# Optimization experiments

Measured on AMD Instinct MI355X. Metric: run time of the kernel, lower is better.

Reference implementation:

```python
import jax, jax.numpy as jnp
import numpy as np

N = 100000      # nodes
E = 1600000     # edges (avg degree 16)
D_IN = 128
CONV_SIZES = [64, 64]
FC_SIZES = [64, 32, 1]


def _glorot(key, shape):
    lim = np.sqrt(6.0 / (shape[0] + shape[1]))
    return jax.random.uniform(key, shape, jnp.float32, -lim, lim)


def setup_inputs() -> dict:
    key = jax.random.key(0)
    ks = jax.random.split(key, 2 + len(CONV_SIZES) + len(FC_SIZES))
    inp = {
        "x": jax.random.normal(ks[0], (N, D_IN), jnp.float32),
        "edge_index": jax.random.randint(ks[1], (2, E), 0, N, dtype=jnp.int64),
    }
    size = D_IN
    ki = 2
    for li, s in enumerate(CONV_SIZES):
        inp[f"cW{li}"] = _glorot(ks[ki], (size, s)); ki += 1
        inp[f"cb{li}"] = jnp.zeros((s,), jnp.float32)
        size = s
    for li, s in enumerate(FC_SIZES):
        inp[f"fW{li}"] = _glorot(ks[ki], (size, s)); ki += 1
        inp[f"fb{li}"] = jnp.zeros((s,), jnp.float32)
        size = s
    return inp


def gcn_conv(x, src, dst, W, b, n_nodes):
    """PyG GCNConv: symmetric normalization with added self-loops."""
    xl = x @ W  # [N, out]
    # degree including self-loop
    deg = jnp.zeros((n_nodes,), xl.dtype).at[dst].add(1.0) + 1.0
    dinv = jax.lax.rsqrt(deg)
    norm = dinv[src] * dinv[dst]                 # [E]
    msg = xl[src] * norm[:, None]                # gather + scale, [E, out]
    agg = jax.ops.segment_sum(msg, dst, num_segments=n_nodes)
    # self-loop contribution: norm = 1/deg
    return agg + xl * (1.0 / deg)[:, None] + b


def reference(x, edge_index, cW0, cb0, cW1, cb1, fW0, fb0, fW1, fb1, fW2, fb2):
    src, dst = edge_index[0], edge_index[1]
    h = jnp.tanh(gcn_conv(x, src, dst, cW0, cb0, N))
    h = jnp.tanh(gcn_conv(h, src, dst, cW1, cb1, N))
    h = jnp.tanh(h @ fW0 + fb0)
    h = jnp.tanh(h @ fW1 + fb1)
    return h @ fW2 + fb2  # [N, 1]
```

## Files before the change

### kernel.cpp

```cpp
#include <hip/hip_runtime.h>
#include <math.h>

#define N_NODES 100000
#define N_EDGES 1600000
#define NB     391
#define CHUNK  4096
#define NBLK_A 391

typedef unsigned short ushort_t;

__device__ inline unsigned short f2bf(float f) {
    unsigned u = __float_as_uint(f);
    unsigned r = (u + 0x7FFFu + ((u >> 16) & 1u)) >> 16;
    return (unsigned short)r;
}
__device__ inline void acc2(float& a0, float& a1, unsigned u) {
    a0 += __uint_as_float(u << 16);
    a1 += __uint_as_float(u & 0xFFFF0000u);
}
__device__ inline float fast_tanh(float x) {
    float e = __expf(2.0f * x);
    return fmaf(-2.0f, __builtin_amdgcn_rcpf(e + 1.0f), 1.0f);
}
__device__ inline void fma4(float4& acc, const float4 a,
                            const float4 w0, const float4 w1,
                            const float4 w2, const float4 w3) {
    acc.x = fmaf(a.x, w0.x, fmaf(a.y, w1.x, fmaf(a.z, w2.x, fmaf(a.w, w3.x, acc.x))));
    acc.y = fmaf(a.x, w0.y, fmaf(a.y, w1.y, fmaf(a.z, w2.y, fmaf(a.w, w3.y, acc.y))));
    acc.z = fmaf(a.x, w0.z, fmaf(a.y, w1.z, fmaf(a.z, w2.z, fmaf(a.w, w3.z, acc.z))));
    acc.w = fmaf(a.x, w0.w, fmaf(a.y, w1.w, fmaf(a.z, w2.w, fmaf(a.w, w3.w, acc.w))));
}
__device__ inline void bf8_to_f32(float* p, uint4 v) {
    p[0] = __uint_as_float(v.x << 16); p[1] = __uint_as_float(v.x & 0xFFFF0000u);
    p[2] = __uint_as_float(v.y << 16); p[3] = __uint_as_float(v.y & 0xFFFF0000u);
    p[4] = __uint_as_float(v.z << 16); p[5] = __uint_as_float(v.z & 0xFFFF0000u);
    p[6] = __uint_as_float(v.w << 16); p[7] = __uint_as_float(v.w & 0xFFFF0000u);
}


__global__ __launch_bounds__(256) void k_count(const int* __restrict__ dst,
                                               unsigned* __restrict__ cnt) {
    __shared__ unsigned h[NB];
    const int tid = threadIdx.x;
    const long e0 = (long)blockIdx.x * CHUNK;
    for (int i = tid; i < NB; i += 256) h[i] = 0u;
    __syncthreads();
    for (int i = tid; i < CHUNK; i += 256) {
        long e = e0 + i;
        if (e < N_EDGES) atomicAdd(&h[((unsigned)dst[e]) >> 8], 1u);
    }
    __syncthreads();
    for (int b = tid; b < NB; b += 256) cnt[b * NBLK_A + blockIdx.x] = h[b];
}

__global__ __launch_bounds__(512) void k_bucket_scan(unsigned* __restrict__ cnt,
                                                     unsigned* __restrict__ btot) {
    __shared__ unsigned s[512];
    const int tid = threadIdx.x;
    const int b = blockIdx.x;
    unsigned v = (tid < NBLK_A) ? cnt[b * NBLK_A + tid] : 0u;
    s[tid] = v;
    __syncthreads();
    for (int o = 1; o < 512; o <<= 1) {
        unsigned t = (tid >= o) ? s[tid - o] : 0u;
        __syncthreads();
        s[tid] += t;
        __syncthreads();
    }
    if (tid < NBLK_A) cnt[b * NBLK_A + tid] = s[tid] - v;
    if (tid == NBLK_A - 1) btot[b] = s[tid];
}

__global__ __launch_bounds__(512) void k_scan_bkt(const unsigned* __restrict__ btot,
                                                  unsigned* __restrict__ bktbase) {
    __shared__ unsigned s[512];
    const int tid = threadIdx.x;
    unsigned v = (tid < NB) ? btot[tid] : 0u;
    s[tid] = v;
    __syncthreads();
    for (int o = 1; o < 512; o <<= 1) {
        unsigned t = (tid >= o) ? s[tid - o] : 0u;
        __syncthreads();
        s[tid] += t;
        __syncthreads();
    }
    if (tid < NB) bktbase[tid] = s[tid] - v;
    if (tid == NB - 1) bktbase[NB] = s[tid];
}

__global__ __launch_bounds__(256) void k_bin(const int* __restrict__ src,
                                             const int* __restrict__ dst,
                                             const unsigned* __restrict__ cnt,
                                             const unsigned* __restrict__ bktbase,
                                             unsigned* __restrict__ binned) {
    __shared__ unsigned cntA[NB];
    __shared__ unsigned excl[NB];
    __shared__ unsigned gbase[NB];
    __shared__ unsigned scanbuf[512];
    __shared__ unsigned data[CHUNK];
    const int tid = threadIdx.x;
    const long e0 = (long)blockIdx.x * CHUNK;

    for (int i = tid; i < NB; i += 256) cntA[i] = 0u;
    __syncthreads();
    for (int i = tid; i < CHUNK; i += 256) {
        long e = e0 + i;
        if (e < N_EDGES) atomicAdd(&cntA[((unsigned)dst[e]) >> 8], 1u);
    }
    __syncthreads();
    scanbuf[tid] = (tid < NB) ? cntA[tid] : 0u;
    scanbuf[tid + 256] = (tid + 256 < NB) ? cntA[tid + 256] : 0u;
    __syncthreads();
    for (int o = 1; o < 512; o <<= 1) {
        unsigned v0 = (tid >= o) ? scanbuf[tid - o] : 0u;
        unsigned v1 = (tid + 256 >= o) ? scanbuf[tid + 256 - o] : 0u;
        __syncthreads();
        scanbuf[tid] += v0;
        scanbuf[tid + 256] += v1;
        __syncthreads();
    }
    for (int b = tid; b < NB; b += 256) {
        excl[b] = scanbuf[b] - cntA[b];
        gbase[b] = bktbase[b] + cnt[b * NBLK_A + blockIdx.x];
    }
    __syncthreads();
    for (int i = tid; i < NB; i += 256) cntA[i] = 0u;
    __syncthreads();
    for (int i = tid; i < CHUNK; i += 256) {
        long e = e0 + i;
        if (e < N_EDGES) {
            unsigned d = (unsigned)dst[e];
            unsigned b = d >> 8;
            unsigned slot = excl[b] + atomicAdd(&cntA[b], 1u);
            data[slot] = (((unsigned)src[e]) << 8) | (d & 255u);
        }
    }
    __syncthreads();
    const int w = tid >> 6, lane = tid & 63;
    for (int b = w; b < NB; b += 4) {
        unsigned c = cntA[b];
        unsigned sb = excl[b], gb = gbase[b];
        for (unsigned k = lane; k < c; k += 64)
            binned[gb + k] = data[sb + k];
    }
}

__global__ __launch_bounds__(256) void k_csr_fill2(const unsigned* __restrict__ binned,
                                                   const unsigned* __restrict__ bktbase,
                                                   unsigned* __restrict__ rowptr,
                                                   float* __restrict__ dinv,
                                                   int* __restrict__ ssrc) {
    __shared__ unsigned cnt[256];
    __shared__ unsigned s[256];
    __shared__ unsigned cur[256];
    const int b = blockIdx.x;
    const int tid = threadIdx.x;
    const int n0 = b * 256;
    const unsigned beg = bktbase[b], end = bktbase[b + 1];
    cnt[tid] = 0u;
    __syncthreads();
    for (unsigned i = beg + tid; i < end; i += 256)
        atomicAdd(&cnt[binned[i] & 255u], 1u);
    __syncthreads();
    const unsigned v = cnt[tid];
    s[tid] = v;
    __syncthreads();
    for (int o = 1; o < 256; o <<= 1) {
        unsigned t = (tid >= o) ? s[tid - o] : 0u;
        __syncthreads();
        s[tid] += t;
        __syncthreads();
    }
    const unsigned excl = s[tid] - v;
    const int node = n0 + tid;
    if (node < N_NODES) {
        rowptr[node] = beg + excl;
        dinv[node] = rsqrtf((float)(v + 1u));
        if (node == N_NODES - 1) rowptr[N_NODES] = end;
    }
    cur[tid] = beg + excl;
    __syncthreads();
    for (unsigned i = beg + tid; i < end; i += 256) {
        unsigned p = binned[i];
        unsigned pos = atomicAdd(&cur[p & 255u], 1u);
        ssrc[pos] = (int)(p >> 8);
    }
}


template<int K>
__global__ __launch_bounds__(256) void k_gemm_bf(const float* __restrict__ A,
                                                 const float* __restrict__ W,
                                                 const float* __restrict__ dinv,
                                                 ushort_t* __restrict__ C) {
    constexpr int OUT = 64;
    constexpr int BR = 64;
    constexpr int LDA = K + 4;
    __shared__ float Wld[K * OUT];
    __shared__ float Ald[BR * LDA];
    const int tid = threadIdx.x;
    const int row0 = blockIdx.x * BR;
    const int nrows = (N_NODES - row0 < BR) ? (N_NODES - row0) : BR;

    {
        const float4* W4 = reinterpret_cast<const float4*>(W);
        float4* Wl4 = reinterpret_cast<float4*>(Wld);
        for (int i = tid; i < K * OUT / 4; i += 256) Wl4[i] = W4[i];
        const float4* A4 = reinterpret_cast<const float4*>(A + (size_t)row0 * K);
        const int nv = nrows * (K / 4);
        for (int i = tid; i < nv; i += 256) {
            int r = i / (K / 4), q = i % (K / 4);
            *reinterpret_cast<float4*>(&Ald[r * LDA + q * 4]) = A4[i];
        }
    }
    __syncthreads();

    const int tr = tid >> 4;
    const int tc = tid & 15;
    const int r0 = tr * 4;
    float4 acc0 = {0,0,0,0}, acc1 = {0,0,0,0}, acc2v = {0,0,0,0}, acc3 = {0,0,0,0};
#pragma unroll 2
    for (int k4 = 0; k4 < K; k4 += 4) {
        const float4 a0 = *reinterpret_cast<const float4*>(&Ald[(r0 + 0) * LDA + k4]);
        const float4 a1 = *reinterpret_cast<const float4*>(&Ald[(r0 + 1) * LDA + k4]);
        const float4 a2 = *reinterpret_cast<const float4*>(&Ald[(r0 + 2) * LDA + k4]);
        const float4 a3 = *reinterpret_cast<const float4*>(&Ald[(r0 + 3) * LDA + k4]);
        const float4 w0 = *reinterpret_cast<const float4*>(&Wld[(k4 + 0) * OUT + tc * 4]);
        const float4 w1 = *reinterpret_cast<const float4*>(&Wld[(k4 + 1) * OUT + tc * 4]);
        const float4 w2 = *reinterpret_cast<const float4*>(&Wld[(k4 + 2) * OUT + tc * 4]);
        const float4 w3 = *reinterpret_cast<const float4*>(&Wld[(k4 + 3) * OUT + tc * 4]);
        fma4(acc0, a0, w0, w1, w2, w3);
        fma4(acc1, a1, w0, w1, w2, w3);
        fma4(acc2v, a2, w0, w1, w2, w3);
        fma4(acc3, a3, w0, w1, w2, w3);
    }
    float4 accs[4] = {acc0, acc1, acc2v, acc3};
#pragma unroll
    for (int i = 0; i < 4; ++i) {
        const int r = r0 + i;
        if (r < nrows) {
            const float di = dinv[row0 + r];
            ushort4 o;
            o.x = f2bf(accs[i].x * di);
            o.y = f2bf(accs[i].y * di);
            o.z = f2bf(accs[i].z * di);
            o.w = f2bf(accs[i].w * di);
            *reinterpret_cast<ushort4*>(&C[(size_t)(row0 + r) * 64 + tc * 4]) = o;
        }
    }
}

__global__ __launch_bounds__(256) void k_gemm_bfin(const ushort_t* __restrict__ A,
                                                   const float* __restrict__ W,
                                                   const float* __restrict__ dinv,
                                                   ushort_t* __restrict__ C) {
    constexpr int K = 64;
    constexpr int OUT = 64;
    constexpr int BR = 64;
    constexpr int LDA = K + 4;
    __shared__ float Wld[K * OUT];
    __shared__ float Ald[BR * LDA];
    const int tid = threadIdx.x;
    const int row0 = blockIdx.x * BR;
    const int nrows = (N_NODES - row0 < BR) ? (N_NODES - row0) : BR;

    {
        const float4* W4 = reinterpret_cast<const float4*>(W);
        float4* Wl4 = reinterpret_cast<float4*>(Wld);
        for (int i = tid; i < K * OUT / 4; i += 256) Wl4[i] = W4[i];
        const uint4* A4 = reinterpret_cast<const uint4*>(A + (size_t)row0 * K);
        const int nv = nrows * 8;
        for (int i = tid; i < nv; i += 256) {
            int r = i >> 3, q = i & 7;
            bf8_to_f32(&Ald[r * LDA + q * 8], A4[i]);
        }
    }
    __syncthreads();

    const int tr = tid >> 4;
    const int tc = tid & 15;
    const int r0 = tr * 4;
    float4 acc0 = {0,0,0,0}, acc1 = {0,0,0,0}, acc2v = {0,0,0,0}, acc3 = {0,0,0,0};
#pragma unroll 2
    for (int k4 = 0; k4 < K; k4 += 4) {
        const float4 a0 = *reinterpret_cast<const float4*>(&Ald[(r0 + 0) * LDA + k4]);
        const float4 a1 = *reinterpret_cast<const float4*>(&Ald[(r0 + 1) * LDA + k4]);
        const float4 a2 = *reinterpret_cast<const float4*>(&Ald[(r0 + 2) * LDA + k4]);
        const float4 a3 = *reinterpret_cast<const float4*>(&Ald[(r0 + 3) * LDA + k4]);
        const float4 w0 = *reinterpret_cast<const float4*>(&Wld[(k4 + 0) * OUT + tc * 4]);
        const float4 w1 = *reinterpret_cast<const float4*>(&Wld[(k4 + 1) * OUT + tc * 4]);
        const float4 w2 = *reinterpret_cast<const float4*>(&Wld[(k4 + 2) * OUT + tc * 4]);
        const float4 w3 = *reinterpret_cast<const float4*>(&Wld[(k4 + 3) * OUT + tc * 4]);
        fma4(acc0, a0, w0, w1, w2, w3);
        fma4(acc1, a1, w0, w1, w2, w3);
        fma4(acc2v, a2, w0, w1, w2, w3);
        fma4(acc3, a3, w0, w1, w2, w3);
    }
    float4 accs[4] = {acc0, acc1, acc2v, acc3};
#pragma unroll
    for (int i = 0; i < 4; ++i) {
        const int r = r0 + i;
        if (r < nrows) {
            const float di = dinv[row0 + r];
            ushort4 o;
            o.x = f2bf(accs[i].x * di);
            o.y = f2bf(accs[i].y * di);
            o.z = f2bf(accs[i].z * di);
            o.w = f2bf(accs[i].w * di);
            *reinterpret_cast<ushort4*>(&C[(size_t)(row0 + r) * 64 + tc * 4]) = o;
        }
    }
}

__global__ __launch_bounds__(256) void k_agg(const ushort_t* __restrict__ xlb,
                                             const float* __restrict__ dinv,
                                             const unsigned* __restrict__ rowptr,
                                             const int* __restrict__ ssrc,
                                             const float* __restrict__ bias,
                                             ushort_t* __restrict__ hb) {
    const int node = blockIdx.x * 4 + (threadIdx.x >> 6);
    const int lane = threadIdx.x & 63;
    const int g = lane >> 3;
    const int l = lane & 7;
    const uint4* xb4 = reinterpret_cast<const uint4*>(xlb);

    const unsigned beg = rowptr[node], end = rowptr[node + 1];
    float a[8] = {0.f,0.f,0.f,0.f,0.f,0.f,0.f,0.f};
    float b[8] = {0.f,0.f,0.f,0.f,0.f,0.f,0.f,0.f};
    if (g == 0) {
        const uint4 v = xb4[(size_t)node * 8 + l];
        acc2(a[0], a[1], v.x); acc2(a[2], a[3], v.y);
        acc2(a[4], a[5], v.z); acc2(a[6], a[7], v.w);
    }
    unsigned j = beg + g;
    for (; j + 8 < end; j += 16) {
        const int s0 = ssrc[j];
        const int s1 = ssrc[j + 8];
        const uint4 v0 = xb4[(size_t)s0 * 8 + l];
        const uint4 v1 = xb4[(size_t)s1 * 8 + l];
        acc2(a[0], a[1], v0.x); acc2(a[2], a[3], v0.y);
        acc2(a[4], a[5], v0.z); acc2(a[6], a[7], v0.w);
        acc2(b[0], b[1], v1.x); acc2(b[2], b[3], v1.y);
        acc2(b[4], b[5], v1.z); acc2(b[6], b[7], v1.w);
    }
    if (j < end) {
        const uint4 v = xb4[(size_t)ssrc[j] * 8 + l];
        acc2(a[0], a[1], v.x); acc2(a[2], a[3], v.y);
        acc2(a[4], a[5], v.z); acc2(a[6], a[7], v.w);
    }
#pragma unroll
    for (int i = 0; i < 8; ++i) a[i] += b[i];
#pragma unroll
    for (int i = 0; i < 8; ++i) {
        a[i] += __shfl_xor(a[i], 8);
        a[i] += __shfl_xor(a[i], 16);
        a[i] += __shfl_xor(a[i], 32);
    }
    if (g == 0) {
        const float di = dinv[node];
        const float4 b0 = reinterpret_cast<const float4*>(bias)[l * 2];
        const float4 b1 = reinterpret_cast<const float4*>(bias)[l * 2 + 1];
        float r0 = fast_tanh(fmaf(a[0], di, b0.x));
        float r1 = fast_tanh(fmaf(a[1], di, b0.y));
        float r2 = fast_tanh(fmaf(a[2], di, b0.z));
        float r3 = fast_tanh(fmaf(a[3], di, b0.w));
        float r4 = fast_tanh(fmaf(a[4], di, b1.x));
        float r5 = fast_tanh(fmaf(a[5], di, b1.y));
        float r6 = fast_tanh(fmaf(a[6], di, b1.z));
        float r7 = fast_tanh(fmaf(a[7], di, b1.w));
        uint4 o;
        o.x = (unsigned)f2bf(r0) | ((unsigned)f2bf(r1) << 16);
        o.y = (unsigned)f2bf(r2) | ((unsigned)f2bf(r3) << 16);
        o.z = (unsigned)f2bf(r4) | ((unsigned)f2bf(r5) << 16);
        o.w = (unsigned)f2bf(r6) | ((unsigned)f2bf(r7) << 16);
        reinterpret_cast<uint4*>(hb)[(size_t)node * 8 + l] = o;
    }
}

__global__ __launch_bounds__(256, 4) void k_fc(const ushort_t* __restrict__ h2,
                                               const float* __restrict__ fW0, const float* __restrict__ fb0,
                                               const float* __restrict__ fW1, const float* __restrict__ fb1,
                                               const float* __restrict__ fW2, const float* __restrict__ fb2,
                                               float* __restrict__ out) {
    constexpr int BR = 32;
    constexpr int LDH = 68;
    __shared__ float W0[64 * 64];
    __shared__ float W1[64 * 32];
    __shared__ float Hin[BR * LDH];
    __shared__ float Ht[BR * LDH];
    __shared__ float Hs[BR * 33];
    __shared__ float W2s[33];
    const int tid = threadIdx.x;
    {
        const float4* w04 = reinterpret_cast<const float4*>(fW0);
        float4* W04 = reinterpret_cast<float4*>(W0);
        for (int i = tid; i < 64 * 16; i += 256) W04[i] = w04[i];
        const float4* w14 = reinterpret_cast<const float4*>(fW1);
        float4* W14 = reinterpret_cast<float4*>(W1);
        for (int i = tid; i < 64 * 8; i += 256) W14[i] = w14[i];
        if (tid < 32) W2s[tid] = fW2[tid];
        if (tid == 32) W2s[32] = fb2[0];
    }
    const long row0 = (long)blockIdx.x * BR;
    {
        const uint4* H4 = reinterpret_cast<const uint4*>(h2 + row0 * 64);
        if (tid < BR * 8) {
            int r = tid >> 3, q = tid & 7;
            bf8_to_f32(&Hin[r * LDH + q * 8], H4[tid]);
        }
    }
    __syncthreads();

    {
        const int rp = tid >> 4;
        const int cq = tid & 15;
        const int r0 = rp * 2, r1 = r0 + 1;
        const float4 bias = reinterpret_cast<const float4*>(fb0)[cq];
        float4 acc0 = bias, acc1 = bias;
#pragma unroll 2
        for (int k4 = 0; k4 < 64; k4 += 4) {
            const float4 a0 = *reinterpret_cast<const float4*>(&Hin[r0 * LDH + k4]);
            const float4 a1 = *reinterpret_cast<const float4*>(&Hin[r1 * LDH + k4]);
            const float4 w0 = *reinterpret_cast<const float4*>(&W0[(k4 + 0) * 64 + cq * 4]);
            const float4 w1 = *reinterpret_cast<const float4*>(&W0[(k4 + 1) * 64 + cq * 4]);
            const float4 w2 = *reinterpret_cast<const float4*>(&W0[(k4 + 2) * 64 + cq * 4]);
            const float4 w3 = *reinterpret_cast<const float4*>(&W0[(k4 + 3) * 64 + cq * 4]);
            fma4(acc0, a0, w0, w1, w2, w3);
            fma4(acc1, a1, w0, w1, w2, w3);
        }
        float4 t0, t1;
        t0.x = fast_tanh(acc0.x); t0.y = fast_tanh(acc0.y);
        t0.z = fast_tanh(acc0.z); t0.w = fast_tanh(acc0.w);
        t1.x = fast_tanh(acc1.x); t1.y = fast_tanh(acc1.y);
        t1.z = fast_tanh(acc1.z); t1.w = fast_tanh(acc1.w);
        *reinterpret_cast<float4*>(&Ht[r0 * LDH + cq * 4]) = t0;
        *reinterpret_cast<float4*>(&Ht[r1 * LDH + cq * 4]) = t1;
    }
    __syncthreads();

    {
        const int r = tid >> 3;
        const int cq = tid & 7;
        const float4 bias = reinterpret_cast<const float4*>(fb1)[cq];
        float4 acc0 = bias;
#pragma unroll 2
        for (int k4 = 0; k4 < 64; k4 += 4) {
            const float4 a0 = *reinterpret_cast<const float4*>(&Ht[r * LDH + k4]);
            const float4 w0 = *reinterpret_cast<const float4*>(&W1[(k4 + 0) * 32 + cq * 4]);
            const float4 w1 = *reinterpret_cast<const float4*>(&W1[(k4 + 1) * 32 + cq * 4]);
            const float4 w2 = *reinterpret_cast<const float4*>(&W1[(k4 + 2) * 32 + cq * 4]);
            const float4 w3 = *reinterpret_cast<const float4*>(&W1[(k4 + 3) * 32 + cq * 4]);
            fma4(acc0, a0, w0, w1, w2, w3);
        }
        Hs[r * 33 + cq * 4 + 0] = fast_tanh(acc0.x);
        Hs[r * 33 + cq * 4 + 1] = fast_tanh(acc0.y);
        Hs[r * 33 + cq * 4 + 2] = fast_tanh(acc0.z);
        Hs[r * 33 + cq * 4 + 3] = fast_tanh(acc0.w);
    }
    __syncthreads();

    if (tid < BR) {
        float a = W2s[32];
        for (int k = 0; k < 32; ++k) a = fmaf(Hs[tid * 33 + k], W2s[k], a);
        out[row0 + tid] = a;
    }
}


extern "C" void kernel_launch(void* const* d_in, const int* in_sizes, int n_in,
                              void* d_out, int out_size, void* d_ws, size_t ws_size,
                              hipStream_t stream) {
    const float* x    = (const float*)d_in[0];
    const int*   eidx = (const int*)d_in[1];
    const float* cW0  = (const float*)d_in[2];
    const float* cb0  = (const float*)d_in[3];
    const float* cW1  = (const float*)d_in[4];
    const float* cb1  = (const float*)d_in[5];
    const float* fW0  = (const float*)d_in[6];
    const float* fb0  = (const float*)d_in[7];
    const float* fW1  = (const float*)d_in[8];
    const float* fb1  = (const float*)d_in[9];
    const float* fW2  = (const float*)d_in[10];
    const float* fb2  = (const float*)d_in[11];
    float* out = (float*)d_out;

    const int* src = eidx;
    const int* dst = eidx + N_EDGES;

    char* ws = (char*)d_ws;
    unsigned* rowptr  = (unsigned*)(ws);
    float*    dinv    = (float*)   (ws + 400016);
    unsigned* cnt     = (unsigned*)(ws + 800016);
    unsigned* btot    = (unsigned*)(ws + 1411552);
    unsigned* bktbase = (unsigned*)(ws + 1413120);
    int*      ssrc    = (int*)     (ws + 1414688);
    ushort_t* xlb     = (ushort_t*)(ws + 7814688);
    unsigned* binned  = (unsigned*)(ws + 20614688);
    ushort_t* hb      = (ushort_t*)(ws + 27014688);

    const int gRow = N_NODES / 32;
    const int gGemm = (N_NODES + 63) / 64;
    const int gAgg = N_NODES / 4;

    k_count<<<NBLK_A, 256, 0, stream>>>(dst, cnt);
    k_bucket_scan<<<NB, 512, 0, stream>>>(cnt, btot);
    k_scan_bkt<<<1, 512, 0, stream>>>(btot, bktbase);
    k_bin<<<NBLK_A, 256, 0, stream>>>(src, dst, cnt, bktbase, binned);
    k_csr_fill2<<<NB, 256, 0, stream>>>(binned, bktbase, rowptr, dinv, ssrc);

    k_gemm_bf<128><<<gGemm, 256, 0, stream>>>(x, cW0, dinv, xlb);
    k_agg<<<gAgg, 256, 0, stream>>>(xlb, dinv, rowptr, ssrc, cb0, hb);
    k_gemm_bfin<<<gGemm, 256, 0, stream>>>(hb, cW1, dinv, xlb);
    k_agg<<<gAgg, 256, 0, stream>>>(xlb, dinv, rowptr, ssrc, cb1, hb);
    k_fc<<<gRow, 256, 0, stream>>>(hb, fW0, fb0, fW1, fb1, fW2, fb2, out);
}
```

Measured before the change: 249.8 us.

## Fuse first GEMM with edge counting and defer degree scaling to aggregation

The first-layer GEMM no longer depends on dinv, so it is launched together with the edge-count histogram in one grid: extra blocks do the counting while the rest compute x@W0. The source-side dinv scaling is moved into a templated aggregation kernel that gathers dinv[src] per edge. The binning kernel now scatters its output with a per-slot bucket index instead of a per-bucket wave loop. This drops one kernel launch and overlaps the GEMM with the CSR build, at the cost of an extra scalar gather per edge in the first aggregation.

```diff
diff --git a/kernel.cpp b/kernel.cpp
--- a/kernel.cpp
+++ b/kernel.cpp
@@ -6,6 +6,7 @@
 #define NB     391
 #define CHUNK  4096
 #define NBLK_A 391
+#define GEMM0_BLOCKS 1563
 
 typedef unsigned short ushort_t;
 
@@ -17,6 +18,10 @@
 __device__ inline void acc2(float& a0, float& a1, unsigned u) {
     a0 += __uint_as_float(u << 16);
     a1 += __uint_as_float(u & 0xFFFF0000u);
+}
+__device__ inline void acc2s(float& a0, float& a1, unsigned u, float s) {
+    a0 = fmaf(__uint_as_float(u << 16), s, a0);
+    a1 = fmaf(__uint_as_float(u & 0xFFFF0000u), s, a1);
 }
 __device__ inline float fast_tanh(float x) {
     float e = __expf(2.0f * x);
@@ -37,171 +42,34 @@
     p[6] = __uint_as_float(v.w << 16); p[7] = __uint_as_float(v.w & 0xFFFF0000u);
 }
 
-
-__global__ __launch_bounds__(256) void k_count(const int* __restrict__ dst,
-                                               unsigned* __restrict__ cnt) {
-    __shared__ unsigned h[NB];
-    const int tid = threadIdx.x;
-    const long e0 = (long)blockIdx.x * CHUNK;
-    for (int i = tid; i < NB; i += 256) h[i] = 0u;
-    __syncthreads();
-    for (int i = tid; i < CHUNK; i += 256) {
-        long e = e0 + i;
-        if (e < N_EDGES) atomicAdd(&h[((unsigned)dst[e]) >> 8], 1u);
-    }
-    __syncthreads();
-    for (int b = tid; b < NB; b += 256) cnt[b * NBLK_A + blockIdx.x] = h[b];
-}
-
-__global__ __launch_bounds__(512) void k_bucket_scan(unsigned* __restrict__ cnt,
-                                                     unsigned* __restrict__ btot) {
-    __shared__ unsigned s[512];
-    const int tid = threadIdx.x;
-    const int b = blockIdx.x;
-    unsigned v = (tid < NBLK_A) ? cnt[b * NBLK_A + tid] : 0u;
-    s[tid] = v;
-    __syncthreads();
-    for (int o = 1; o < 512; o <<= 1) {
-        unsigned t = (tid >= o) ? s[tid - o] : 0u;
-        __syncthreads();
-        s[tid] += t;
-        __syncthreads();
-    }
-    if (tid < NBLK_A) cnt[b * NBLK_A + tid] = s[tid] - v;
-    if (tid == NBLK_A - 1) btot[b] = s[tid];
-}
-
-__global__ __launch_bounds__(512) void k_scan_bkt(const unsigned* __restrict__ btot,
-                                                  unsigned* __restrict__ bktbase) {
-    __shared__ unsigned s[512];
-    const int tid = threadIdx.x;
-    unsigned v = (tid < NB) ? btot[tid] : 0u;
-    s[tid] = v;
-    __syncthreads();
-    for (int o = 1; o < 512; o <<= 1) {
-        unsigned t = (tid >= o) ? s[tid - o] : 0u;
-        __syncthreads();
-        s[tid] += t;
-        __syncthreads();
-    }
-    if (tid < NB) bktbase[tid] = s[tid] - v;
-    if (tid == NB - 1) bktbase[NB] = s[tid];
-}
-
-__global__ __launch_bounds__(256) void k_bin(const int* __restrict__ src,
-                                             const int* __restrict__ dst,
-                                             const unsigned* __restrict__ cnt,
-                                             const unsigned* __restrict__ bktbase,
-                                             unsigned* __restrict__ binned) {
-    __shared__ unsigned cntA[NB];
-    __shared__ unsigned excl[NB];
-    __shared__ unsigned gbase[NB];
-    __shared__ unsigned scanbuf[512];
-    __shared__ unsigned data[CHUNK];
-    const int tid = threadIdx.x;
-    const long e0 = (long)blockIdx.x * CHUNK;
-
-    for (int i = tid; i < NB; i += 256) cntA[i] = 0u;
-    __syncthreads();
-    for (int i = tid; i < CHUNK; i += 256) {
-        long e = e0 + i;
-        if (e < N_EDGES) atomicAdd(&cntA[((unsigned)dst[e]) >> 8], 1u);
-    }
-    __syncthreads();
-    scanbuf[tid] = (tid < NB) ? cntA[tid] : 0u;
-    scanbuf[tid + 256] = (tid + 256 < NB) ? cntA[tid + 256] : 0u;
-    __syncthreads();
-    for (int o = 1; o < 512; o <<= 1) {
-        unsigned v0 = (tid >= o) ? scanbuf[tid - o] : 0u;
-        unsigned v1 = (tid + 256 >= o) ? scanbuf[tid + 256 - o] : 0u;
-        __syncthreads();
-        scanbuf[tid] += v0;
-        scanbuf[tid + 256] += v1;
-        __syncthreads();
-    }
-    for (int b = tid; b < NB; b += 256) {
-        excl[b] = scanbuf[b] - cntA[b];
-        gbase[b] = bktbase[b] + cnt[b * NBLK_A + blockIdx.x];
-    }
-    __syncthreads();
-    for (int i = tid; i < NB; i += 256) cntA[i] = 0u;
-    __syncthreads();
-    for (int i = tid; i < CHUNK; i += 256) {
-        long e = e0 + i;
-        if (e < N_EDGES) {
-            unsigned d = (unsigned)dst[e];
-            unsigned b = d >> 8;
-            unsigned slot = excl[b] + atomicAdd(&cntA[b], 1u);
-            data[slot] = (((unsigned)src[e]) << 8) | (d & 255u);
-        }
-    }
-    __syncthreads();
-    const int w = tid >> 6, lane = tid & 63;
-    for (int b = w; b < NB; b += 4) {
-        unsigned c = cntA[b];
-        unsigned sb = excl[b], gb = gbase[b];
-        for (unsigned k = lane; k < c; k += 64)
-            binned[gb + k] = data[sb + k];
-    }
-}
-
-__global__ __launch_bounds__(256) void k_csr_fill2(const unsigned* __restrict__ binned,
-                                                   const unsigned* __restrict__ bktbase,
-                                                   unsigned* __restrict__ rowptr,
-                                                   float* __restrict__ dinv,
-                                                   int* __restrict__ ssrc) {
-    __shared__ unsigned cnt[256];
-    __shared__ unsigned s[256];
-    __shared__ unsigned cur[256];
-    const int b = blockIdx.x;
-    const int tid = threadIdx.x;
-    const int n0 = b * 256;
-    const unsigned beg = bktbase[b], end = bktbase[b + 1];
-    cnt[tid] = 0u;
-    __syncthreads();
-    for (unsigned i = beg + tid; i < end; i += 256)
-        atomicAdd(&cnt[binned[i] & 255u], 1u);
-    __syncthreads();
-    const unsigned v = cnt[tid];
-    s[tid] = v;
-    __syncthreads();
-    for (int o = 1; o < 256; o <<= 1) {
-        unsigned t = (tid >= o) ? s[tid - o] : 0u;
-        __syncthreads();
-        s[tid] += t;
-        __syncthreads();
-    }
-    const unsigned excl = s[tid] - v;
-    const int node = n0 + tid;
-    if (node < N_NODES) {
-        rowptr[node] = beg + excl;
-        dinv[node] = rsqrtf((float)(v + 1u));
-        if (node == N_NODES - 1) rowptr[N_NODES] = end;
-    }
-    cur[tid] = beg + excl;
-    __syncthreads();
-    for (unsigned i = beg + tid; i < end; i += 256) {
-        unsigned p = binned[i];
-        unsigned pos = atomicAdd(&cur[p & 255u], 1u);
-        ssrc[pos] = (int)(p >> 8);
-    }
-}
-
-
-template<int K>
-__global__ __launch_bounds__(256) void k_gemm_bf(const float* __restrict__ A,
-                                                 const float* __restrict__ W,
-                                                 const float* __restrict__ dinv,
-                                                 ushort_t* __restrict__ C) {
-    constexpr int OUT = 64;
-    constexpr int BR = 64;
-    constexpr int LDA = K + 4;
-    __shared__ float Wld[K * OUT];
-    __shared__ float Ald[BR * LDA];
-    const int tid = threadIdx.x;
+__global__ __launch_bounds__(256) void k_gemm0_count(const float* __restrict__ A,
+                                                     const float* __restrict__ W,
+                                                     ushort_t* __restrict__ C,
+                                                     const int* __restrict__ dst,
+                                                     unsigned* __restrict__ cnt) {
+    constexpr int K = 128, OUT = 64, BR = 64, LDA = K + 4;
+    __shared__ __align__(16) char smem[(K * OUT + BR * LDA) * 4];
+    const int tid = threadIdx.x;
+
+    if (blockIdx.x >= GEMM0_BLOCKS) {
+        unsigned* h = (unsigned*)smem;
+        const int cb = blockIdx.x - GEMM0_BLOCKS;
+        const long e0 = (long)cb * CHUNK;
+        for (int i = tid; i < NB; i += 256) h[i] = 0u;
+        __syncthreads();
+        for (int i = tid; i < CHUNK; i += 256) {
+            long e = e0 + i;
+            if (e < N_EDGES) atomicAdd(&h[((unsigned)dst[e]) >> 8], 1u);
+        }
+        __syncthreads();
+        for (int b = tid; b < NB; b += 256) cnt[b * NBLK_A + cb] = h[b];
+        return;
+    }
+
+    float* Wld = (float*)smem;
+    float* Ald = Wld + K * OUT;
     const int row0 = blockIdx.x * BR;
     const int nrows = (N_NODES - row0 < BR) ? (N_NODES - row0) : BR;
-
     {
         const float4* W4 = reinterpret_cast<const float4*>(W);
         float4* Wl4 = reinterpret_cast<float4*>(Wld);
@@ -215,8 +83,7 @@
     }
     __syncthreads();
 
-    const int tr = tid >> 4;
-    const int tc = tid & 15;
+    const int tr = tid >> 4, tc = tid & 15;
     const int r0 = tr * 4;
     float4 acc0 = {0,0,0,0}, acc1 = {0,0,0,0}, acc2v = {0,0,0,0}, acc3 = {0,0,0,0};
 #pragma unroll 2
@@ -239,25 +106,151 @@
     for (int i = 0; i < 4; ++i) {
         const int r = r0 + i;
         if (r < nrows) {
-            const float di = dinv[row0 + r];
             ushort4 o;
-            o.x = f2bf(accs[i].x * di);
-            o.y = f2bf(accs[i].y * di);
-            o.z = f2bf(accs[i].z * di);
-            o.w = f2bf(accs[i].w * di);
+            o.x = f2bf(accs[i].x); o.y = f2bf(accs[i].y);
+            o.z = f2bf(accs[i].z); o.w = f2bf(accs[i].w);
             *reinterpret_cast<ushort4*>(&C[(size_t)(row0 + r) * 64 + tc * 4]) = o;
         }
     }
 }
+
+
+__global__ __launch_bounds__(512) void k_bucket_scan(unsigned* __restrict__ cnt,
+                                                     unsigned* __restrict__ btot) {
+    __shared__ unsigned s[512];
+    const int tid = threadIdx.x;
+    const int b = blockIdx.x;
+    unsigned v = (tid < NBLK_A) ? cnt[b * NBLK_A + tid] : 0u;
+    s[tid] = v;
+    __syncthreads();
+    for (int o = 1; o < 512; o <<= 1) {
+        unsigned t = (tid >= o) ? s[tid - o] : 0u;
+        __syncthreads();
+        s[tid] += t;
+        __syncthreads();
+    }
+    if (tid < NBLK_A) cnt[b * NBLK_A + tid] = s[tid] - v;
+    if (tid == NBLK_A - 1) btot[b] = s[tid];
+}
+
+__global__ __launch_bounds__(512) void k_scan_bkt(const unsigned* __restrict__ btot,
+                                                  unsigned* __restrict__ bktbase) {
+    __shared__ unsigned s[512];
+    const int tid = threadIdx.x;
+    unsigned v = (tid < NB) ? btot[tid] : 0u;
+    s[tid] = v;
+    __syncthreads();
+    for (int o = 1; o < 512; o <<= 1) {
+        unsigned t = (tid >= o) ? s[tid - o] : 0u;
+        __syncthreads();
+        s[tid] += t;
+        __syncthreads();
+    }
+    if (tid < NB) bktbase[tid] = s[tid] - v;
+    if (tid == NB - 1) bktbase[NB] = s[tid];
+}
+
+__global__ __launch_bounds__(256) void k_bin(const int* __restrict__ src,
+                                             const int* __restrict__ dst,
+                                             const unsigned* __restrict__ cnt,
+                                             const unsigned* __restrict__ bktbase,
+                                             unsigned* __restrict__ binned) {
+    __shared__ unsigned cntA[NB];
+    __shared__ unsigned excl[NB];
+    __shared__ unsigned gbase[NB];
+    __shared__ unsigned scanbuf[512];
+    __shared__ unsigned data[CHUNK];
+    __shared__ ushort_t bkt16[CHUNK];
+    const int tid = threadIdx.x;
+    const long e0 = (long)blockIdx.x * CHUNK;
+    const int n = (N_EDGES - e0 < CHUNK) ? (int)(N_EDGES - e0) : CHUNK;
+
+    for (int i = tid; i < NB; i += 256) cntA[i] = 0u;
+    __syncthreads();
+    for (int i = tid; i < n; i += 256)
+        atomicAdd(&cntA[((unsigned)dst[e0 + i]) >> 8], 1u);
+    __syncthreads();
+    scanbuf[tid] = (tid < NB) ? cntA[tid] : 0u;
+    scanbuf[tid + 256] = (tid + 256 < NB) ? cntA[tid + 256] : 0u;
+    __syncthreads();
+    for (int o = 1; o < 512; o <<= 1) {
+        unsigned v0 = (tid >= o) ? scanbuf[tid - o] : 0u;
+        unsigned v1 = (tid + 256 >= o) ? scanbuf[tid + 256 - o] : 0u;
+        __syncthreads();
+        scanbuf[tid] += v0;
+        scanbuf[tid + 256] += v1;
+        __syncthreads();
+    }
+    for (int b = tid; b < NB; b += 256) {
+        excl[b] = scanbuf[b] - cntA[b];
+        gbase[b] = bktbase[b] + cnt[b * NBLK_A + blockIdx.x];
+    }
+    __syncthreads();
+    for (int i = tid; i < NB; i += 256) cntA[i] = 0u;
+    __syncthreads();
+    for (int i = tid; i < n; i += 256) {
+        long e = e0 + i;
+        unsigned d = (unsigned)dst[e];
+        unsigned b = d >> 8;
+        unsigned slot = excl[b] + atomicAdd(&cntA[b], 1u);
+        data[slot] = (((unsigned)src[e]) << 8) | (d & 255u);
+        bkt16[slot] = (ushort_t)b;
+    }
+    __syncthreads();
+    for (int i = tid; i < n; i += 256) {
+        unsigned b = bkt16[i];
+        binned[gbase[b] + (unsigned)i - excl[b]] = data[i];
+    }
+}
+
+__global__ __launch_bounds__(256) void k_csr_fill2(const unsigned* __restrict__ binned,
+                                                   const unsigned* __restrict__ bktbase,
+                                                   unsigned* __restrict__ rowptr,
+                                                   float* __restrict__ dinv,
+                                                   int* __restrict__ ssrc) {
+    __shared__ unsigned cnt[256];
+    __shared__ unsigned s[256];
+    __shared__ unsigned cur[256];
+    const int b = blockIdx.x;
+    const int tid = threadIdx.x;
+    const int n0 = b * 256;
+    const unsigned beg = bktbase[b], end = bktbase[b + 1];
+    cnt[tid] = 0u;
+    __syncthreads();
+    for (unsigned i = beg + tid; i < end; i += 256)
+        atomicAdd(&cnt[binned[i] & 255u], 1u);
+    __syncthreads();
+    const unsigned v = cnt[tid];
+    s[tid] = v;
+    __syncthreads();
+    for (int o = 1; o < 256; o <<= 1) {
+        unsigned t = (tid >= o) ? s[tid - o] : 0u;
+        __syncthreads();
+        s[tid] += t;
+        __syncthreads();
+    }
+    const unsigned excl = s[tid] - v;
+    const int node = n0 + tid;
+    if (node < N_NODES) {
+        rowptr[node] = beg + excl;
+        dinv[node] = rsqrtf((float)(v + 1u));
+        if (node == N_NODES - 1) rowptr[N_NODES] = end;
+    }
+    cur[tid] = beg + excl;
+    __syncthreads();
+    for (unsigned i = beg + tid; i < end; i += 256) {
+        unsigned p = binned[i];
+        unsigned pos = atomicAdd(&cur[p & 255u], 1u);
+        ssrc[pos] = (int)(p >> 8);
+    }
+}
+
 
 __global__ __launch_bounds__(256) void k_gemm_bfin(const ushort_t* __restrict__ A,
                                                    const float* __restrict__ W,
                                                    const float* __restrict__ dinv,
                                                    ushort_t* __restrict__ C) {
-    constexpr int K = 64;
-    constexpr int OUT = 64;
-    constexpr int BR = 64;
-    constexpr int LDA = K + 4;
+    constexpr int K = 64, OUT = 64, BR = 64, LDA = K + 4;
     __shared__ float Wld[K * OUT];
     __shared__ float Ald[BR * LDA];
     const int tid = threadIdx.x;
@@ -277,8 +270,7 @@
     }
     __syncthreads();
 
-    const int tr = tid >> 4;
-    const int tc = tid & 15;
+    const int tr = tid >> 4, tc = tid & 15;
     const int r0 = tr * 4;
     float4 acc0 = {0,0,0,0}, acc1 = {0,0,0,0}, acc2v = {0,0,0,0}, acc3 = {0,0,0,0};
 #pragma unroll 2
@@ -312,6 +304,7 @@
     }
 }
 
+template<bool SCALED_IN>
 __global__ __launch_bounds__(256) void k_agg(const ushort_t* __restrict__ xlb,
                                              const float* __restrict__ dinv,
                                              const unsigned* __restrict__ rowptr,
@@ -329,8 +322,14 @@
     float b[8] = {0.f,0.f,0.f,0.f,0.f,0.f,0.f,0.f};
     if (g == 0) {
         const uint4 v = xb4[(size_t)node * 8 + l];
-        acc2(a[0], a[1], v.x); acc2(a[2], a[3], v.y);
-        acc2(a[4], a[5], v.z); acc2(a[6], a[7], v.w);
+        if (SCALED_IN) {
+            acc2(a[0], a[1], v.x); acc2(a[2], a[3], v.y);
+            acc2(a[4], a[5], v.z); acc2(a[6], a[7], v.w);
+        } else {
+            const float dn = dinv[node];
+            acc2s(a[0], a[1], v.x, dn); acc2s(a[2], a[3], v.y, dn);
+            acc2s(a[4], a[5], v.z, dn); acc2s(a[6], a[7], v.w, dn);
+        }
     }
     unsigned j = beg + g;
     for (; j + 8 < end; j += 16) {
@@ -338,15 +337,31 @@
         const int s1 = ssrc[j + 8];
         const uint4 v0 = xb4[(size_t)s0 * 8 + l];
         const uint4 v1 = xb4[(size_t)s1 * 8 + l];
-        acc2(a[0], a[1], v0.x); acc2(a[2], a[3], v0.y);
-        acc2(a[4], a[5], v0.z); acc2(a[6], a[7], v0.w);
-        acc2(b[0], b[1], v1.x); acc2(b[2], b[3], v1.y);
-        acc2(b[4], b[5], v1.z); acc2(b[6], b[7], v1.w);
+        if (SCALED_IN) {
+            acc2(a[0], a[1], v0.x); acc2(a[2], a[3], v0.y);
+            acc2(a[4], a[5], v0.z); acc2(a[6], a[7], v0.w);
+            acc2(b[0], b[1], v1.x); acc2(b[2], b[3], v1.y);
+            acc2(b[4], b[5], v1.z); acc2(b[6], b[7], v1.w);
+        } else {
+            const float d0 = dinv[s0];
+            const float d1 = dinv[s1];
+            acc2s(a[0], a[1], v0.x, d0); acc2s(a[2], a[3], v0.y, d0);
+            acc2s(a[4], a[5], v0.z, d0); acc2s(a[6], a[7], v0.w, d0);
+            acc2s(b[0], b[1], v1.x, d1); acc2s(b[2], b[3], v1.y, d1);
+            acc2s(b[4], b[5], v1.z, d1); acc2s(b[6], b[7], v1.w, d1);
+        }
     }
     if (j < end) {
-        const uint4 v = xb4[(size_t)ssrc[j] * 8 + l];
-        acc2(a[0], a[1], v.x); acc2(a[2], a[3], v.y);
-        acc2(a[4], a[5], v.z); acc2(a[6], a[7], v.w);
+        const int s0 = ssrc[j];
+        const uint4 v = xb4[(size_t)s0 * 8 + l];
+        if (SCALED_IN) {
+            acc2(a[0], a[1], v.x); acc2(a[2], a[3], v.y);
+            acc2(a[4], a[5], v.z); acc2(a[6], a[7], v.w);
+        } else {
+            const float d0 = dinv[s0];
+            acc2s(a[0], a[1], v.x, d0); acc2s(a[2], a[3], v.y, d0);
+            acc2s(a[4], a[5], v.z, d0); acc2s(a[6], a[7], v.w, d0);
+        }
     }
 #pragma unroll
     for (int i = 0; i < 8; ++i) a[i] += b[i];
@@ -502,15 +517,14 @@
     const int gGemm = (N_NODES + 63) / 64;
     const int gAgg = N_NODES / 4;
 
-    k_count<<<NBLK_A, 256, 0, stream>>>(dst, cnt);
+    k_gemm0_count<<<GEMM0_BLOCKS + NBLK_A, 256, 0, stream>>>(x, cW0, xlb, dst, cnt);
     k_bucket_scan<<<NB, 512, 0, stream>>>(cnt, btot);
     k_scan_bkt<<<1, 512, 0, stream>>>(btot, bktbase);
     k_bin<<<NBLK_A, 256, 0, stream>>>(src, dst, cnt, bktbase, binned);
     k_csr_fill2<<<NB, 256, 0, stream>>>(binned, bktbase, rowptr, dinv, ssrc);
 
-    k_gemm_bf<128><<<gGemm, 256, 0, stream>>>(x, cW0, dinv, xlb);
-    k_agg<<<gAgg, 256, 0, stream>>>(xlb, dinv, rowptr, ssrc, cb0, hb);
+    k_agg<false><<<gAgg, 256, 0, stream>>>(xlb, dinv, rowptr, ssrc, cb0, hb);
     k_gemm_bfin<<<gGemm, 256, 0, stream>>>(hb, cW1, dinv, xlb);
-    k_agg<<<gAgg, 256, 0, stream>>>(xlb, dinv, rowptr, ssrc, cb1, hb);
+    k_agg<true><<<gAgg, 256, 0, stream>>>(xlb, dinv, rowptr, ssrc, cb1, hb);
     k_fc<<<gRow, 256, 0, stream>>>(hb, fW0, fb0, fW1, fb1, fW2, fb2, out);
 }
```

Result: faster. 231.0 us (-7.5%).
